# Kernel optimization log

Measured on AMD Instinct MI355X. Metric: run time of the kernel, lower is better.

Reference implementation:

```python
import jax, jax.numpy as jnp
import numpy as np


def _seg_softmax(e, seg, n):
    m = jax.ops.segment_max(e, seg, num_segments=n)
    ex = jnp.exp(e - m[seg])
    s = jax.ops.segment_sum(ex, seg, num_segments=n)
    return ex / (s[seg] + 1e-16)


def _gat_conv(x, src, dst, ea, W, a_s, a_d, We, a_e, b, heads, C, concat, N):
    # PyG GATConv math (eval mode, no dropout)
    h = (x @ W).reshape(N, heads, C)                    # [N,H,C]
    he = (ea @ We).reshape(-1, heads, C)                # [Ef,H,C]
    al = jnp.sum(h * a_s, -1)[src] + jnp.sum(h * a_d, -1)[dst] + jnp.sum(he * a_e, -1)
    al = jax.nn.leaky_relu(al, 0.2)                     # [Ef,H]
    alpha = _seg_softmax(al, dst, N)
    out = jax.ops.segment_sum(alpha[:, :, None] * h[src], dst, num_segments=N)
    out = out.reshape(N, heads * C) if concat else out.mean(1)
    return out + b


def _ln(x, g, b):
    mu = x.mean(-1, keepdims=True)
    v = x.var(-1, keepdims=True)
    return (x - mu) / jnp.sqrt(v + 1e-5) * g + b


def setup_inputs() -> dict:
    key = jax.random.key(0)
    ks = jax.random.split(key, 20)
    B, L, E_PER = 512, 64, 4
    N = B * L
    E = N * E_PER
    x = jax.random.normal(ks[0], (N, 55), jnp.float32)
    # within-graph random edges (each graph is a contiguous block of L nodes)
    off = (jnp.arange(E) // (L * E_PER)) * L
    src = off + jax.random.randint(ks[1], (E,), 0, L)
    dst = off + jax.random.randint(ks[2], (E,), 0, L)
    edge_index = jnp.stack([src, dst])
    edge_attr = jax.random.uniform(ks[3], (E, 6), dtype=jnp.float32)
    node_gid = jnp.arange(N) // L
    food_ids = jax.random.randint(ks[4], (B,), 0, 29)
    p = lambda i, shape: jax.random.normal(ks[i], shape, jnp.float32) * 0.05
    return dict(
        x=x, edge_attr=edge_attr, edge_index=edge_index, node_gid=node_gid, food_ids=food_ids,
        W1=p(5, (55, 1024)), as1=p(6, (4, 256)), ad1=p(7, (4, 256)),
        We1=p(8, (6, 1024)), ae1=p(9, (4, 256)), b1=jnp.zeros((1024,), jnp.float32),
        g1=jnp.ones((1024,), jnp.float32), be1=jnp.zeros((1024,), jnp.float32),
        W2=p(10, (1024, 256)), as2=p(11, (1, 256)), ad2=p(12, (1, 256)),
        We2=p(13, (6, 256)), ae2=p(14, (1, 256)), b2=jnp.zeros((256,), jnp.float32),
        g2=jnp.ones((256,), jnp.float32), be2=jnp.zeros((256,), jnp.float32),
        Wa=p(15, (256, 256)), va=p(16, (256,)), emb=p(17, (29, 256)))


def reference(x, edge_attr, edge_index, node_gid, food_ids,
              W1, as1, ad1, We1, ae1, b1, g1, be1,
              W2, as2, ad2, We2, ae2, b2, g2, be2,
              Wa, va, emb):
    N = x.shape[0]
    B = food_ids.shape[0]
    src, dst = edge_index[0], edge_index[1]
    # add self loops; self-loop edge_attr = mean of incoming edge attrs (PyG fill_value='mean')
    ones = jnp.ones((src.shape[0],), x.dtype)
    deg = jax.ops.segment_sum(ones, dst, num_segments=N)
    mean_ea = jax.ops.segment_sum(edge_attr, dst, num_segments=N) / jnp.maximum(deg, 1.0)[:, None]
    loop = jnp.arange(N)
    src_f = jnp.concatenate([src, loop])
    dst_f = jnp.concatenate([dst, loop])
    ea_f = jnp.concatenate([edge_attr, mean_ea], 0)
    # GATEncoder
    h = _gat_conv(x, src_f, dst_f, ea_f, W1, as1, ad1, We1, ae1, b1, 4, 256, True, N)
    h = jax.nn.relu(_ln(h, g1, be1))
    h = _gat_conv(h, src_f, dst_f, ea_f, W2, as2, ad2, We2, ae2, b2, 1, 256, False, N)
    h = _ln(h, g2, be2)                                  # [N,256]
    # per-graph attention over nodes, then attention-weighted max-pool
    scores = jnp.tanh(h @ Wa) @ va                       # [N]
    attn = _seg_softmax(scores, node_gid, B)             # [N]
    hw = h * attn[:, None]
    drug_fea = jax.ops.segment_max(hw, node_gid, num_segments=B)[:, None, :]  # [B,1,256]
    food_fea = emb[food_ids][:, None, :]                 # [B,1,256]
    return drug_fea, food_fea, attn
```

## Files before the change

### kernel.cpp

```cpp
#include <hip/hip_runtime.h>
#include <cstdint>
#include <cstddef>


#define LEAKY_SLOPE 0.2f

typedef __attribute__((ext_vector_type(8))) _Float16 half8;
typedef __attribute__((ext_vector_type(4))) float facc4;

__global__ void k_prep_w(const float* __restrict__ W1, const float* __restrict__ W2,
                         const float* __restrict__ Wa,
                         const float* __restrict__ We1, const float* __restrict__ ae1,
                         const float* __restrict__ We2, const float* __restrict__ ae2,
                         const float* __restrict__ as1, const float* __restrict__ ad1,
                         _Float16* __restrict__ w1f, _Float16* __restrict__ w2t,
                         _Float16* __restrict__ wat, float* __restrict__ fold) {
    int idx = blockIdx.x * blockDim.x + threadIdx.x;
    if (idx < 1024 * 64) {
        int head = idx >> 14;
        int rem = idx & 16383;
        int c = rem >> 6, k = rem & 63;
        _Float16 v = (k < 55) ? (_Float16)W1[(size_t)k * 1024 + head * 256 + c]
                              : (_Float16)0.f;
        int dst = head * 16384 + ((c >> 4) * 2 + (k >> 5)) * 512 +
                  ((c & 15) + 16 * ((k >> 3) & 3)) * 8 + (k & 7);
        w1f[dst] = v;
        return;
    }
    idx -= 1024 * 64;
    if (idx < 256 * 1024) {
        int c = idx >> 10, k = idx & 1023;
        w2t[idx] = (_Float16)W2[(size_t)k * 256 + c];
        return;
    }
    idx -= 256 * 1024;
    if (idx < 256 * 256) {
        int c = idx >> 8, k = idx & 255;
        int dst = ((c >> 4) * 8 + (k >> 5)) * 512 + ((c & 15) + 16 * ((k >> 3) & 3)) * 8 + (k & 7);
        wat[dst] = (_Float16)Wa[(size_t)k * 256 + c];
        return;
    }
    int t = idx - 256 * 256;
    if (t < 24) {
        int k = t >> 2, h = t & 3;
        float s = 0.f;
        for (int c = 0; c < 256; ++c) s += We1[k * 1024 + h * 256 + c] * ae1[h * 256 + c];
        fold[t] = s;
    } else if (t < 30) {
        int k = t - 24;
        float s = 0.f;
        for (int c = 0; c < 256; ++c) s += We2[k * 256 + c] * ae2[c];
        fold[32 + k] = s;
    } else if (t >= 64 && t < 284) {
        int i = t - 64, k = i >> 2, h = i & 3;
        float s = 0.f;
        for (int c = 0; c < 256; ++c) s += W1[k * 1024 + h * 256 + c] * as1[h * 256 + c];
        fold[64 + i] = s;
    } else if (t >= 320 && t < 540) {
        int i = t - 320, k = i >> 2, h = i & 3;
        float s = 0.f;
        for (int c = 0; c < 256; ++c) s += W1[k * 1024 + h * 256 + c] * ad1[h * 256 + c];
        fold[320 + i] = s;
    }
}

__global__ void k_prep_x(const float* __restrict__ x, const float* __restrict__ wa1,
                         const float* __restrict__ wd1, _Float16* __restrict__ xbf,
                         float* __restrict__ ss1, float* __restrict__ sd1, int N) {
    int idx = blockIdx.x * blockDim.x + threadIdx.x;
    if (idx < N * 64) {
        int n = idx >> 6, k = idx & 63;
        _Float16 v = (k < 55) ? (_Float16)x[(size_t)n * 55 + k] : (_Float16)0.f;
        int g = n >> 6, nl = n & 63;
        size_t dst = (size_t)g * 4096 +
                     (((k >> 4) * 2 + (nl >> 5)) * 512 +
                      ((k & 15) + 16 * ((nl >> 3) & 3)) * 8 + (nl & 7));
        xbf[dst] = v;
        return;
    }
    int n = idx - N * 64;
    if (n >= N) return;
    float a0 = 0, a1 = 0, a2 = 0, a3 = 0, d0 = 0, d1 = 0, d2 = 0, d3 = 0;
    for (int k = 0; k < 55; ++k) {
        float xv = x[(size_t)n * 55 + k];
        float4 wa = *reinterpret_cast<const float4*>(&wa1[k * 4]);
        float4 wd = *reinterpret_cast<const float4*>(&wd1[k * 4]);
        a0 += xv * wa.x; a1 += xv * wa.y; a2 += xv * wa.z; a3 += xv * wa.w;
        d0 += xv * wd.x; d1 += xv * wd.y; d2 += xv * wd.z; d3 += xv * wd.w;
    }
    *reinterpret_cast<float4*>(&ss1[n * 4]) = make_float4(a0, a1, a2, a3);
    *reinterpret_cast<float4*>(&sd1[n * 4]) = make_float4(d0, d1, d2, d3);
}

__global__ __launch_bounds__(256) void k_graph_csr(
    const int* __restrict__ ei, const float* __restrict__ ea,
    const float* __restrict__ we1, const float* __restrict__ we2,
    int* __restrict__ coff, int* __restrict__ eid,
    float* __restrict__ ead1, float* __restrict__ ead2, int E, int B) {
    __shared__ int degL[64];
    __shared__ float meaL[64][6];
    __shared__ int cs[65];
    __shared__ int fillL[64];
    int g = blockIdx.x;
    int ng = g * 64;
    int e0 = g * 256;
    int tid = threadIdx.x;
    if (tid < 64) {
        degL[tid] = 0; fillL[tid] = 0;
#pragma unroll
        for (int k = 0; k < 6; ++k) meaL[tid][k] = 0.f;
    }
    __syncthreads();
    int eg = e0 + tid;
    int dst = ei[E + eg];
    int dl = dst - ng;
    atomicAdd(&degL[dl], 1);
#pragma unroll
    for (int k = 0; k < 6; ++k) atomicAdd(&meaL[dl][k], ea[(size_t)eg * 6 + k]);
    __syncthreads();
    if (tid < 64) {
        int v = degL[tid] + 1;
        int incl = v;
#pragma unroll
        for (int o = 1; o < 64; o <<= 1) {
            int up = __shfl_up(incl, o);
            if (tid >= o) incl += up;
        }
        cs[tid + 1] = incl;
        if (tid == 0) cs[0] = 0;
        coff[ng + tid] = g * 320 + (incl - v);
        if (g == B - 1 && tid == 63) coff[ng + 64] = (g + 1) * 320;
    }
    __syncthreads();
    {
        float v[4] = {};
        float v2 = 0.f;
        const float* eap = ea + (size_t)eg * 6;
#pragma unroll
        for (int k = 0; k < 6; ++k) {
            float a = eap[k];
#pragma unroll
            for (int h = 0; h < 4; ++h) v[h] += a * we1[k * 4 + h];
            v2 += a * we2[k];
        }
#pragma unroll
        for (int h = 0; h < 4; ++h) ead1[(size_t)eg * 4 + h] = v[h];
        ead2[eg] = v2;
        int pos = cs[dl] + atomicAdd(&fillL[dl], 1);
        eid[g * 320 + pos] = eg;
    }
    if (tid < 64) {
        float inv = 1.f / fmaxf((float)degL[tid], 1.f);
        float v[4] = {};
        float v2 = 0.f;
#pragma unroll
        for (int k = 0; k < 6; ++k) {
            float a = meaL[tid][k] * inv;
#pragma unroll
            for (int h = 0; h < 4; ++h) v[h] += a * we1[k * 4 + h];
            v2 += a * we2[k];
        }
        int se = E + ng + tid;
#pragma unroll
        for (int h = 0; h < 4; ++h) ead1[(size_t)se * 4 + h] = v[h];
        ead2[se] = v2;
        int pos = cs[tid] + atomicAdd(&fillL[tid], 1);
        eid[g * 320 + pos] = se;
    }
}

__global__ __launch_bounds__(512) void k_layer1(
    const _Float16* __restrict__ xbf,
    const int* __restrict__ coff, const int* __restrict__ eid, const int* __restrict__ ei,
    const float* __restrict__ ead1, const float* __restrict__ ss1,
    const float* __restrict__ sd1,
    const _Float16* __restrict__ w1f, _Float16* __restrict__ hpre,
    int E, int g0) {
    __shared__ _Float16 Pm[4][4096];
    __shared__ float llds[384][4];
    __shared__ int slds[384];
    _Float16* XAf = &Pm[0][0];
    int g = blockIdx.x;
    int ng = (g0 + g) * 64;
    int tid = threadIdx.x;
    int lane = tid & 63, wid = tid >> 6;
    int l15 = lane & 15, l4 = lane >> 4;
    for (int i = tid; i < 4 * 4096 / 8; i += 512)
        *reinterpret_cast<int4*>(&Pm[0][0] + i * 8) = int4{0, 0, 0, 0};
    int pbase = coff[ng];
    int pcnt = coff[ng + 64] - pbase;
    if (pcnt > 384) pcnt = 384;
    for (int p = tid; p < pcnt; p += 512) {
        int e = eid[pbase + p];
        int s, d;
        if (e < E) { s = ei[e]; d = ei[E + e]; } else { s = e - E; d = s; }
        slds[p] = s - ng;
        float4 sv = *reinterpret_cast<const float4*>(&ss1[s * 4]);
        float4 dv = *reinterpret_cast<const float4*>(&sd1[d * 4]);
        float4 ev = *reinterpret_cast<const float4*>(&ead1[(size_t)e * 4]);
        float v0 = sv.x + dv.x + ev.x, v1 = sv.y + dv.y + ev.y;
        float v2 = sv.z + dv.z + ev.z, v3 = sv.w + dv.w + ev.w;
        llds[p][0] = (v0 > 0.f) ? v0 : LEAKY_SLOPE * v0;
        llds[p][1] = (v1 > 0.f) ? v1 : LEAKY_SLOPE * v1;
        llds[p][2] = (v2 > 0.f) ? v2 : LEAKY_SLOPE * v2;
        llds[p][3] = (v3 > 0.f) ? v3 : LEAKY_SLOPE * v3;
    }
    __syncthreads();
    if (tid < 256) {
        int dst = tid >> 2, h = tid & 3;
        int p0 = coff[ng + dst] - pbase, p1 = coff[ng + dst + 1] - pbase;
        float m = -1e30f;
        for (int p = p0; p < p1; ++p) m = fmaxf(m, llds[p][h]);
        float sm = 0.f;
        for (int p = p0; p < p1; ++p) sm += expf(llds[p][h] - m);
        float iv = 1.f / (sm + 1e-16f);
        for (int p = p0; p < p1; ++p) {
            int src = slds[p];
            int pos = dst * 64 + (((src >> 3) ^ (dst & 7)) << 3) + (src & 7);
            Pm[h][pos] = (_Float16)((float)Pm[h][pos] + expf(llds[p][h] - m) * iv);
        }
    }
    __syncthreads();
    int head = wid >> 1, fjh = wid & 1;
    const _Float16* xg = xbf + (size_t)(g0 + g) * 4096;
    facc4 acc1[4][2] = {};
#pragma unroll
    for (int kk = 0; kk < 2; ++kk) {
        half8 af[4], bf[2];
#pragma unroll
        for (int f = 0; f < 4; ++f) {
            int arow = f * 16 + l15;
            af[f] = *reinterpret_cast<const half8*>(
                &Pm[head][arow * 64 + (((kk * 4 + l4) ^ (arow & 7)) << 3)]);
        }
#pragma unroll
        for (int f = 0; f < 2; ++f)
            bf[f] = *reinterpret_cast<const half8*>(
                xg + (((fjh * 2 + f) * 2 + kk) * 512 + lane * 8));
#pragma unroll
        for (int fi = 0; fi < 4; ++fi)
#pragma unroll
            for (int fj = 0; fj < 2; ++fj)
                acc1[fi][fj] = __builtin_amdgcn_mfma_f32_16x16x32_f16(
                    af[fi], bf[fj], acc1[fi][fj], 0, 0, 0);
    }
    __syncthreads();
#pragma unroll
    for (int fi = 0; fi < 4; ++fi)
#pragma unroll
        for (int fj = 0; fj < 2; ++fj)
#pragma unroll
            for (int i = 0; i < 4; ++i) {
                int rl = l4 * 4 + i;
                int dst = head * 4096 + (fi * 2 + fjh) * 512 +
                          ((fj * 2 + (l15 >> 3)) * 16 + rl) * 8 + (l15 & 7);
                XAf[dst] = (_Float16)acc1[fi][fj][i];
            }
    __syncthreads();
    int hw = wid >> 1, ch = wid & 1;
    facc4 acc2[4][8] = {};
#pragma unroll
    for (int kk = 0; kk < 2; ++kk) {
        half8 af[4], bf[8];
#pragma unroll
        for (int f = 0; f < 4; ++f)
            af[f] = *reinterpret_cast<const half8*>(
                &XAf[hw * 4096 + (f * 2 + kk) * 512 + lane * 8]);
#pragma unroll
        for (int f = 0; f < 8; ++f)
            bf[f] = *reinterpret_cast<const half8*>(
                w1f + hw * 16384 + ((ch * 8 + f) * 2 + kk) * 512 + lane * 8);
#pragma unroll
        for (int fi = 0; fi < 4; ++fi)
#pragma unroll
            for (int fj = 0; fj < 8; ++fj)
                acc2[fi][fj] = __builtin_amdgcn_mfma_f32_16x16x32_f16(
                    af[fi], bf[fj], acc2[fi][fj], 0, 0, 0);
    }
#pragma unroll
    for (int fi = 0; fi < 4; ++fi)
#pragma unroll
        for (int fj = 0; fj < 8; ++fj)
#pragma unroll
            for (int i = 0; i < 4; ++i) {
                int r = g * 64 + fi * 16 + l4 * 4 + i;
                int cc = hw * 256 + ch * 128 + fj * 16 + l15;
                hpre[(size_t)r * 1024 + cc] = (_Float16)acc2[fi][fj][i];
            }
}

__global__ __launch_bounds__(256) void k_ln1(
    const _Float16* __restrict__ hpre, const float* __restrict__ b1,
    const float* __restrict__ g1, const float* __restrict__ be1,
    _Float16* __restrict__ hln) {
    int row = blockIdx.x * 4 + (threadIdx.x >> 6);
    int lane = threadIdx.x & 63;
    const _Float16* src = hpre + (size_t)row * 1024;
    float v[16];
    half8 h0 = *reinterpret_cast<const half8*>(src + lane * 8);
    half8 h1 = *reinterpret_cast<const half8*>(src + 512 + lane * 8);
    float lsum = 0.f, lsq = 0.f;
#pragma unroll
    for (int j = 0; j < 8; ++j) {
        v[j] = (float)h0[j] + b1[lane * 8 + j];
        v[8 + j] = (float)h1[j] + b1[512 + lane * 8 + j];
    }
#pragma unroll
    for (int j = 0; j < 16; ++j) { lsum += v[j]; lsq += v[j] * v[j]; }
    for (int o = 32; o; o >>= 1) { lsum += __shfl_xor(lsum, o); lsq += __shfl_xor(lsq, o); }
    float mu = lsum * (1.f / 1024.f);
    float var = lsq * (1.f / 1024.f) - mu * mu;
    float rstd = rsqrtf(var + 1e-5f);
    half8 o0, o1;
#pragma unroll
    for (int j = 0; j < 8; ++j) {
        int c = lane * 8 + j;
        o0[j] = (_Float16)fmaxf((v[j] - mu) * rstd * g1[c] + be1[c], 0.f);
    }
#pragma unroll
    for (int j = 0; j < 8; ++j) {
        int c = 512 + lane * 8 + j;
        o1[j] = (_Float16)fmaxf((v[8 + j] - mu) * rstd * g1[c] + be1[c], 0.f);
    }
    *reinterpret_cast<half8*>(hln + (size_t)row * 1024 + lane * 8) = o0;
    *reinterpret_cast<half8*>(hln + (size_t)row * 1024 + 512 + lane * 8) = o1;
}

__global__ __launch_bounds__(512) void k_gemm2(
    const _Float16* __restrict__ A, const _Float16* __restrict__ BT,
    _Float16* __restrict__ h2f) {
    __shared__ _Float16 As[128 * 64];
    __shared__ _Float16 Bs[256 * 64];
    int tid = threadIdx.x;
    int lane = tid & 63, wid = tid >> 6;
    int wr = wid >> 2, wc = wid & 3;
    int l15 = lane & 15, l4 = lane >> 4;
    int r0 = blockIdx.x * 128;
    facc4 acc[4][4] = {};
    for (int kt = 0; kt < 1024; kt += 64) {
#pragma unroll
        for (int i = 0; i < 2; ++i) {
            int ch = tid + 512 * i;
            int row = ch >> 3, col16 = ch & 7;
            int sw = col16 ^ (row & 7);
            *reinterpret_cast<int4*>(&As[row * 64 + sw * 8]) =
                *reinterpret_cast<const int4*>(A + (size_t)(r0 + row) * 1024 + kt + col16 * 8);
        }
#pragma unroll
        for (int i = 0; i < 4; ++i) {
            int ch = tid + 512 * i;
            int row = ch >> 3, col16 = ch & 7;
            int sw = col16 ^ (row & 7);
            *reinterpret_cast<int4*>(&Bs[row * 64 + sw * 8]) =
                *reinterpret_cast<const int4*>(BT + (size_t)row * 1024 + kt + col16 * 8);
        }
        __syncthreads();
#pragma unroll
        for (int kk = 0; kk < 2; ++kk) {
            half8 af[4], bf[4];
#pragma unroll
            for (int f = 0; f < 4; ++f) {
                int arow = wr * 64 + f * 16 + l15;
                int ac = (kk * 4 + l4) ^ (arow & 7);
                af[f] = *reinterpret_cast<const half8*>(&As[arow * 64 + ac * 8]);
                int brow = wc * 64 + f * 16 + l15;
                int bc = (kk * 4 + l4) ^ (brow & 7);
                bf[f] = *reinterpret_cast<const half8*>(&Bs[brow * 64 + bc * 8]);
            }
#pragma unroll
            for (int fi = 0; fi < 4; ++fi)
#pragma unroll
                for (int fj = 0; fj < 4; ++fj)
                    acc[fi][fj] = __builtin_amdgcn_mfma_f32_16x16x32_f16(
                        af[fi], bf[fj], acc[fi][fj], 0, 0, 0);
        }
        __syncthreads();
    }
#pragma unroll
    for (int fi = 0; fi < 4; ++fi)
#pragma unroll
        for (int fj = 0; fj < 4; ++fj)
#pragma unroll
            for (int i = 0; i < 4; ++i) {
                int r = r0 + wr * 64 + fi * 16 + l4 * 4 + i;
                int cc = wc * 64 + fj * 16 + l15;
                int g = r >> 6, nl = r & 63;
                size_t dst = (size_t)g * 16384 +
                             (((cc >> 4) * 2 + (nl >> 5)) * 512 +
                              ((cc & 15) + 16 * ((nl >> 3) & 3)) * 8 + (nl & 7));
                h2f[dst] = (_Float16)acc[fi][fj][i];
            }
}

__global__ __launch_bounds__(512) void k_graph2f(
    const _Float16* __restrict__ h2f,
    const int* __restrict__ coff, const int* __restrict__ eid, const int* __restrict__ ei,
    const float* __restrict__ ead2, const float* __restrict__ as2,
    const float* __restrict__ ad2,
    const float* __restrict__ b2, const float* __restrict__ g2,
    const float* __restrict__ be2,
    const _Float16* __restrict__ wat, const float* __restrict__ va,
    const int* __restrict__ food, const float* __restrict__ emb,
    float* __restrict__ out, int E, int B, int g0) {
    __shared__ _Float16 hfL[64 * 256];
    _Float16* Pm = hfL;
    float* llds = reinterpret_cast<float*>(hfL + 4096);
    int* slds = reinterpret_cast<int*>(hfL + 4096 + 768);
    __shared__ float rsum[64], rsq[64], ss2L[64], sd2L[64];
    __shared__ float part[8][64];
    __shared__ float at[64];
    int g = blockIdx.x;
    int b = g0 + g;
    int ng = (g0 + g) * 64;
    int tid = threadIdx.x;
    int lane = tid & 63, wid = tid >> 6;
    int l15 = lane & 15, l4 = lane >> 4;
    int cbase = wid * 32;
    if (tid < 64) { rsum[tid] = 0.f; rsq[tid] = 0.f; ss2L[tid] = 0.f; sd2L[tid] = 0.f; }
    for (int i = tid; i < 64 * 64 / 8; i += 512)
        *reinterpret_cast<int4*>(&Pm[0] + i * 8) = int4{0, 0, 0, 0};
    __syncthreads();
    const _Float16* hg = h2f + (size_t)g * 16384;
    half8 bfr[2][2];
#pragma unroll
    for (int kk = 0; kk < 2; ++kk)
#pragma unroll
        for (int f = 0; f < 2; ++f)
            bfr[kk][f] = *reinterpret_cast<const half8*>(
                hg + ((((cbase + f * 16) >> 4) * 2 + kk) * 512 + lane * 8));
    float ps[2][8] = {}, pd[2][8] = {};
#pragma unroll
    for (int kk = 0; kk < 2; ++kk)
#pragma unroll
        for (int f = 0; f < 2; ++f) {
            int c = cbase + f * 16 + l15;
            float a2 = as2[c], d2 = ad2[c];
#pragma unroll
            for (int j = 0; j < 8; ++j) {
                float hv = (float)bfr[kk][f][j];
                ps[kk][j] += hv * a2;
                pd[kk][j] += hv * d2;
            }
        }
#pragma unroll
    for (int kk = 0; kk < 2; ++kk)
#pragma unroll
        for (int j = 0; j < 8; ++j) {
            float s = ps[kk][j], d = pd[kk][j];
            s += __shfl_xor(s, 1); d += __shfl_xor(d, 1);
            s += __shfl_xor(s, 2); d += __shfl_xor(d, 2);
            s += __shfl_xor(s, 4); d += __shfl_xor(d, 4);
            s += __shfl_xor(s, 8); d += __shfl_xor(d, 8);
            if (l15 == 0) {
                int n = kk * 32 + l4 * 8 + j;
                atomicAdd(&ss2L[n], s);
                atomicAdd(&sd2L[n], d);
            }
        }
    __syncthreads();
    int pbase = coff[ng];
    int pcnt = coff[ng + 64] - pbase;
    if (pcnt > 384) pcnt = 384;
    for (int p = tid; p < pcnt; p += 512) {
        int e = eid[pbase + p];
        int s, d;
        if (e < E) { s = ei[e]; d = ei[E + e]; } else { s = e - E; d = s; }
        slds[p] = s - ng;
        float v = ss2L[s - ng] + sd2L[d - ng] + ead2[e];
        llds[p] = (v > 0.f) ? v : LEAKY_SLOPE * v;
    }
    __syncthreads();
    if (tid < 64) {
        int dst = tid;
        int p0 = coff[ng + dst] - pbase, p1 = coff[ng + dst + 1] - pbase;
        float m = -1e30f;
        for (int p = p0; p < p1; ++p) m = fmaxf(m, llds[p]);
        float sm = 0.f;
        for (int p = p0; p < p1; ++p) sm += expf(llds[p] - m);
        float iv = 1.f / (sm + 1e-16f);
        for (int p = p0; p < p1; ++p) {
            int src = slds[p];
            int pos = dst * 64 + (((src >> 3) ^ (dst & 7)) << 3) + (src & 7);
            Pm[pos] = (_Float16)((float)Pm[pos] + expf(llds[p] - m) * iv);
        }
    }
    __syncthreads();
    facc4 acc[4][2] = {};
#pragma unroll
    for (int kk = 0; kk < 2; ++kk) {
        half8 af[4];
#pragma unroll
        for (int f = 0; f < 4; ++f) {
            int arow = f * 16 + l15;
            af[f] = *reinterpret_cast<const half8*>(
                &Pm[arow * 64 + (((kk * 4 + l4) ^ (arow & 7)) << 3)]);
        }
#pragma unroll
        for (int fi = 0; fi < 4; ++fi)
#pragma unroll
            for (int fj = 0; fj < 2; ++fj)
                acc[fi][fj] = __builtin_amdgcn_mfma_f32_16x16x32_f16(
                    af[fi], bfr[kk][fj], acc[fi][fj], 0, 0, 0);
    }
    float bb[2];
#pragma unroll
    for (int fj = 0; fj < 2; ++fj) bb[fj] = b2[cbase + fj * 16 + l15];
#pragma unroll
    for (int fi = 0; fi < 4; ++fi)
#pragma unroll
        for (int i = 0; i < 4; ++i) {
            float s = 0.f, q = 0.f;
#pragma unroll
            for (int fj = 0; fj < 2; ++fj) {
                float v = acc[fi][fj][i] + bb[fj];
                acc[fi][fj][i] = v;
                s += v; q += v * v;
            }
            s += __shfl_xor(s, 1); q += __shfl_xor(q, 1);
            s += __shfl_xor(s, 2); q += __shfl_xor(q, 2);
            s += __shfl_xor(s, 4); q += __shfl_xor(q, 4);
            s += __shfl_xor(s, 8); q += __shfl_xor(q, 8);
            if (l15 == 0) {
                int r = fi * 16 + l4 * 4 + i;
                atomicAdd(&rsum[r], s);
                atomicAdd(&rsq[r], q);
            }
        }
    __syncthreads();
#pragma unroll
    for (int fi = 0; fi < 4; ++fi)
#pragma unroll
        for (int i = 0; i < 4; ++i) {
            int rl = l4 * 4 + i;
            float mu = rsum[fi * 16 + rl] * (1.f / 256.f);
            float var = rsq[fi * 16 + rl] * (1.f / 256.f) - mu * mu;
            float rstd = rsqrtf(var + 1e-5f);
#pragma unroll
            for (int fj = 0; fj < 2; ++fj) {
                int c = cbase + fj * 16 + l15;
                float v = (acc[fi][fj][i] - mu) * rstd * g2[c] + be2[c];
                acc[fi][fj][i] = v;
                int idx = (fi * 8 + wid) * 512 +
                          ((fj * 2 + (l15 >> 3)) * 16 + rl) * 8 + (l15 & 7);
                hfL[idx] = (_Float16)v;
            }
        }
    __syncthreads();
    facc4 acc2[4][2] = {};
#pragma unroll
    for (int kk = 0; kk < 8; ++kk) {
        half8 af[4], bf[2];
#pragma unroll
        for (int f = 0; f < 4; ++f)
            af[f] = *reinterpret_cast<const half8*>(&hfL[(f * 8 + kk) * 512 + lane * 8]);
#pragma unroll
        for (int f = 0; f < 2; ++f)
            bf[f] = *reinterpret_cast<const half8*>(
                wat + (((wid * 2 + f) * 8 + kk) * 512 + lane * 8));
#pragma unroll
        for (int fi = 0; fi < 4; ++fi)
#pragma unroll
            for (int fj = 0; fj < 2; ++fj)
                acc2[fi][fj] = __builtin_amdgcn_mfma_f32_16x16x32_f16(
                    af[fi], bf[fj], acc2[fi][fj], 0, 0, 0);
    }
    float vac[2];
#pragma unroll
    for (int fj = 0; fj < 2; ++fj) vac[fj] = va[cbase + fj * 16 + l15];
#pragma unroll
    for (int fi = 0; fi < 4; ++fi)
#pragma unroll
        for (int i = 0; i < 4; ++i) {
            float v = tanhf(acc2[fi][0][i]) * vac[0] + tanhf(acc2[fi][1][i]) * vac[1];
            v += __shfl_xor(v, 1); v += __shfl_xor(v, 2);
            v += __shfl_xor(v, 4); v += __shfl_xor(v, 8);
            if (l15 == 0) part[wid][fi * 16 + l4 * 4 + i] = v;
        }
    __syncthreads();
    if (tid < 64) {
        float sc = part[0][tid] + part[1][tid] + part[2][tid] + part[3][tid] +
                   part[4][tid] + part[5][tid] + part[6][tid] + part[7][tid];
        float m = sc;
        for (int o = 32; o; o >>= 1) m = fmaxf(m, __shfl_xor(m, o));
        float ex = expf(sc - m);
        float s = ex;
        for (int o = 32; o; o >>= 1) s += __shfl_xor(s, o);
        float a = ex / (s + 1e-16f);
        at[tid] = a;
        out[(size_t)B * 512 + (size_t)b * 64 + tid] = a;
    }
    __syncthreads();
#pragma unroll
    for (int fj = 0; fj < 2; ++fj) {
        float m = -1e30f;
#pragma unroll
        for (int fi = 0; fi < 4; ++fi)
#pragma unroll
            for (int i = 0; i < 4; ++i) {
                int r = fi * 16 + l4 * 4 + i;
                m = fmaxf(m, acc[fi][fj][i] * at[r]);
            }
        m = fmaxf(m, __shfl_xor(m, 16));
        m = fmaxf(m, __shfl_xor(m, 32));
        if (l4 == 0)
            out[(size_t)b * 256 + cbase + fj * 16 + l15] = m;
    }
    if (tid < 256)
        out[(size_t)B * 256 + (size_t)b * 256 + tid] =
            emb[(size_t)food[b] * 256 + tid];
}

extern "C" void kernel_launch(void* const* d_in, const int* in_sizes, int n_in,
                              void* d_out, int out_size, void* d_ws, size_t ws_size,
                              hipStream_t stream) {
    const float* x   = (const float*)d_in[0];
    const float* ea  = (const float*)d_in[1];
    const int*   ei  = (const int*)d_in[2];
    const int*   food= (const int*)d_in[4];
    const float* W1  = (const float*)d_in[5];
    const float* as1 = (const float*)d_in[6];
    const float* ad1 = (const float*)d_in[7];
    const float* We1 = (const float*)d_in[8];
    const float* ae1 = (const float*)d_in[9];
    const float* b1  = (const float*)d_in[10];
    const float* g1  = (const float*)d_in[11];
    const float* be1 = (const float*)d_in[12];
    const float* W2  = (const float*)d_in[13];
    const float* as2 = (const float*)d_in[14];
    const float* ad2 = (const float*)d_in[15];
    const float* We2 = (const float*)d_in[16];
    const float* ae2 = (const float*)d_in[17];
    const float* b2  = (const float*)d_in[18];
    const float* g2  = (const float*)d_in[19];
    const float* be2 = (const float*)d_in[20];
    const float* Wa  = (const float*)d_in[21];
    const float* va  = (const float*)d_in[22];
    const float* emb = (const float*)d_in[23];
    float* out = (float*)d_out;

    const int N  = in_sizes[0] / 55;
    const int E  = in_sizes[2] / 2;
    const int B  = in_sizes[4];
    const int Ef = E + N;
    const int LPG = N / B;

    char* w = (char*)d_ws;
    size_t off = 0;
    auto take = [&](size_t bytes) -> char* {
        char* p = w + off;
        off = (off + bytes + 255) & ~(size_t)255;
        return p;
    };
    int*      coff = (int*)take((size_t)(N + 1) * 4);
    int*      eid  = (int*)take((size_t)Ef * 4);
    float*    ead1 = (float*)take((size_t)Ef * 4 * 4);
    float*    ead2 = (float*)take((size_t)Ef * 4);
    float*    fold = (float*)take(4096 * 4);
    float*    ss1  = (float*)take((size_t)N * 4 * 4);
    float*    sd1  = (float*)take((size_t)N * 4 * 4);
    _Float16* xbf  = (_Float16*)take((size_t)N * 64 * 2);
    _Float16* w1f  = (_Float16*)take((size_t)1024 * 64 * 2);
    _Float16* w2t  = (_Float16*)take((size_t)256 * 1024 * 2);
    _Float16* wat  = (_Float16*)take((size_t)256 * 256 * 2);
    size_t smallEnd = off;

    int G = B;
    while (G > 2 && smallEnd + 2ull * G * 131072 + 768 > ws_size) G >>= 1;
    _Float16* hpre = (_Float16*)take((size_t)G * 131072);
    _Float16* hln  = (_Float16*)take((size_t)G * 131072);
    _Float16* h2f  = (_Float16*)hpre;

    k_prep_w<<<(1024 * 64 + 256 * 1024 + 256 * 256 + 3072 + 255) / 256, 256, 0, stream>>>(
        W1, W2, Wa, We1, ae1, We2, ae2, as1, ad1, w1f, w2t, wat, fold);
    k_prep_x<<<(N * 64 + N + 255) / 256, 256, 0, stream>>>(
        x, fold + 64, fold + 320, xbf, ss1, sd1, N);
    k_graph_csr<<<B, 256, 0, stream>>>(ei, ea, fold, fold + 32, coff, eid,
                                       ead1, ead2, E, B);

    for (int g0 = 0; g0 < B; g0 += G) {
        int Gc = (g0 + G <= B) ? G : (B - g0);
        int NC = Gc * LPG;
        k_layer1<<<Gc, 512, 0, stream>>>(xbf, coff, eid, ei, ead1, ss1, sd1,
                                         w1f, hpre, E, g0);
        k_ln1<<<NC / 4, 256, 0, stream>>>(hpre, b1, g1, be1, hln);
        k_gemm2<<<NC / 128, 512, 0, stream>>>(hln, w2t, h2f);
        k_graph2f<<<Gc, 512, 0, stream>>>(h2f, coff, eid, ei, ead2, as2, ad2,
                                          b2, g2, be2, wat, va, food, emb,
                                          out, E, B, g0);
    }
}
```

Baseline: 148.5 us.

## Fuse bias+LayerNorm+ReLU into layer1 epilogue and store MFMA-fragment layout for gemm2

Layer-1's epilogue now adds the bias, reduces row sums and sums of squares across waves through shared-memory atomics, and applies LayerNorm and ReLU in registers. It writes the result in the fragment-packed layout that gemm2 reads directly from global memory. This removes the separate k_ln1 kernel, one fp16 round trip of the 1024-wide activation, and gemm2's A-tile staging in shared memory. The costs are scattered 2-byte stores in the epilogue, an extra barrier, and gemm2 A loads that go uncached straight from global.

```diff
diff --git a/kernel.cpp b/kernel.cpp
--- a/kernel.cpp
+++ b/kernel.cpp
@@ -174,17 +174,21 @@
     const int* __restrict__ coff, const int* __restrict__ eid, const int* __restrict__ ei,
     const float* __restrict__ ead1, const float* __restrict__ ss1,
     const float* __restrict__ sd1,
-    const _Float16* __restrict__ w1f, _Float16* __restrict__ hpre,
-    int E, int g0) {
+    const _Float16* __restrict__ w1f,
+    const float* __restrict__ b1, const float* __restrict__ g1,
+    const float* __restrict__ be1,
+    _Float16* __restrict__ hlnf, int E, int g0) {
     __shared__ _Float16 Pm[4][4096];
     __shared__ float llds[384][4];
     __shared__ int slds[384];
+    __shared__ float rsum[64], rsq[64];
     _Float16* XAf = &Pm[0][0];
     int g = blockIdx.x;
     int ng = (g0 + g) * 64;
     int tid = threadIdx.x;
     int lane = tid & 63, wid = tid >> 6;
     int l15 = lane & 15, l4 = lane >> 4;
+    if (tid < 64) { rsum[tid] = 0.f; rsq[tid] = 0.f; }
     for (int i = tid; i < 4 * 4096 / 8; i += 512)
         *reinterpret_cast<int4*>(&Pm[0][0] + i * 8) = int4{0, 0, 0, 0};
     int pbase = coff[ng];
@@ -258,6 +262,7 @@
             }
     __syncthreads();
     int hw = wid >> 1, ch = wid & 1;
+    int cbase = hw * 256 + ch * 128;
     facc4 acc2[4][8] = {};
 #pragma unroll
     for (int kk = 0; kk < 2; ++kk) {
@@ -277,75 +282,64 @@
                 acc2[fi][fj] = __builtin_amdgcn_mfma_f32_16x16x32_f16(
                     af[fi], bf[fj], acc2[fi][fj], 0, 0, 0);
     }
+    float bb[8];
+#pragma unroll
+    for (int fj = 0; fj < 8; ++fj) bb[fj] = b1[cbase + fj * 16 + l15];
 #pragma unroll
     for (int fi = 0; fi < 4; ++fi)
 #pragma unroll
-        for (int fj = 0; fj < 8; ++fj)
-#pragma unroll
-            for (int i = 0; i < 4; ++i) {
-                int r = g * 64 + fi * 16 + l4 * 4 + i;
-                int cc = hw * 256 + ch * 128 + fj * 16 + l15;
-                hpre[(size_t)r * 1024 + cc] = (_Float16)acc2[fi][fj][i];
-            }
+        for (int i = 0; i < 4; ++i) {
+            float s = 0.f, q = 0.f;
+#pragma unroll
+            for (int fj = 0; fj < 8; ++fj) {
+                float v = acc2[fi][fj][i] + bb[fj];
+                acc2[fi][fj][i] = v;
+                s += v; q += v * v;
+            }
+            s += __shfl_xor(s, 1); q += __shfl_xor(q, 1);
+            s += __shfl_xor(s, 2); q += __shfl_xor(q, 2);
+            s += __shfl_xor(s, 4); q += __shfl_xor(q, 4);
+            s += __shfl_xor(s, 8); q += __shfl_xor(q, 8);
+            if (l15 == 0) {
+                int r = fi * 16 + l4 * 4 + i;
+                atomicAdd(&rsum[r], s);
+                atomicAdd(&rsq[r], q);
+            }
+        }
+    __syncthreads();
+#pragma unroll
+    for (int fi = 0; fi < 4; ++fi)
+#pragma unroll
+        for (int i = 0; i < 4; ++i) {
+            int rl = l4 * 4 + i;
+            int r = fi * 16 + rl;
+            float mu = rsum[r] * (1.f / 1024.f);
+            float var = rsq[r] * (1.f / 1024.f) - mu * mu;
+            float rstd = rsqrtf(var + 1e-5f);
+#pragma unroll
+            for (int fj = 0; fj < 8; ++fj) {
+                int c = cbase + fj * 16 + l15;
+                float v = fmaxf((acc2[fi][fj][i] - mu) * rstd * g1[c] + be1[c], 0.f);
+                size_t dst = (size_t)g * 65536 +
+                             ((fi * 32 + (c >> 5)) * 512 +
+                              (rl + 16 * ((c >> 3) & 3)) * 8 + (c & 7));
+                hlnf[dst] = (_Float16)v;
+            }
+        }
 }
 
-__global__ __launch_bounds__(256) void k_ln1(
-    const _Float16* __restrict__ hpre, const float* __restrict__ b1,
-    const float* __restrict__ g1, const float* __restrict__ be1,
-    _Float16* __restrict__ hln) {
-    int row = blockIdx.x * 4 + (threadIdx.x >> 6);
-    int lane = threadIdx.x & 63;
-    const _Float16* src = hpre + (size_t)row * 1024;
-    float v[16];
-    half8 h0 = *reinterpret_cast<const half8*>(src + lane * 8);
-    half8 h1 = *reinterpret_cast<const half8*>(src + 512 + lane * 8);
-    float lsum = 0.f, lsq = 0.f;
-#pragma unroll
-    for (int j = 0; j < 8; ++j) {
-        v[j] = (float)h0[j] + b1[lane * 8 + j];
-        v[8 + j] = (float)h1[j] + b1[512 + lane * 8 + j];
-    }
-#pragma unroll
-    for (int j = 0; j < 16; ++j) { lsum += v[j]; lsq += v[j] * v[j]; }
-    for (int o = 32; o; o >>= 1) { lsum += __shfl_xor(lsum, o); lsq += __shfl_xor(lsq, o); }
-    float mu = lsum * (1.f / 1024.f);
-    float var = lsq * (1.f / 1024.f) - mu * mu;
-    float rstd = rsqrtf(var + 1e-5f);
-    half8 o0, o1;
-#pragma unroll
-    for (int j = 0; j < 8; ++j) {
-        int c = lane * 8 + j;
-        o0[j] = (_Float16)fmaxf((v[j] - mu) * rstd * g1[c] + be1[c], 0.f);
-    }
-#pragma unroll
-    for (int j = 0; j < 8; ++j) {
-        int c = 512 + lane * 8 + j;
-        o1[j] = (_Float16)fmaxf((v[8 + j] - mu) * rstd * g1[c] + be1[c], 0.f);
-    }
-    *reinterpret_cast<half8*>(hln + (size_t)row * 1024 + lane * 8) = o0;
-    *reinterpret_cast<half8*>(hln + (size_t)row * 1024 + 512 + lane * 8) = o1;
-}
-
 __global__ __launch_bounds__(512) void k_gemm2(
-    const _Float16* __restrict__ A, const _Float16* __restrict__ BT,
+    const _Float16* __restrict__ hlnf, const _Float16* __restrict__ BT,
     _Float16* __restrict__ h2f) {
-    __shared__ _Float16 As[128 * 64];
     __shared__ _Float16 Bs[256 * 64];
     int tid = threadIdx.x;
     int lane = tid & 63, wid = tid >> 6;
     int wr = wid >> 2, wc = wid & 3;
     int l15 = lane & 15, l4 = lane >> 4;
     int r0 = blockIdx.x * 128;
+    const _Float16* Ag = hlnf + (size_t)(r0 / 64 + wr) * 65536;
     facc4 acc[4][4] = {};
     for (int kt = 0; kt < 1024; kt += 64) {
-#pragma unroll
-        for (int i = 0; i < 2; ++i) {
-            int ch = tid + 512 * i;
-            int row = ch >> 3, col16 = ch & 7;
-            int sw = col16 ^ (row & 7);
-            *reinterpret_cast<int4*>(&As[row * 64 + sw * 8]) =
-                *reinterpret_cast<const int4*>(A + (size_t)(r0 + row) * 1024 + kt + col16 * 8);
-        }
 #pragma unroll
         for (int i = 0; i < 4; ++i) {
             int ch = tid + 512 * i;
@@ -357,12 +351,12 @@
         __syncthreads();
 #pragma unroll
         for (int kk = 0; kk < 2; ++kk) {
+            int ks = (kt >> 5) + kk;
             half8 af[4], bf[4];
 #pragma unroll
             for (int f = 0; f < 4; ++f) {
-                int arow = wr * 64 + f * 16 + l15;
-                int ac = (kk * 4 + l4) ^ (arow & 7);
-                af[f] = *reinterpret_cast<const half8*>(&As[arow * 64 + ac * 8]);
+                af[f] = *reinterpret_cast<const half8*>(
+                    Ag + (f * 32 + ks) * 512 + lane * 8);
                 int brow = wc * 64 + f * 16 + l15;
                 int bc = (kk * 4 + l4) ^ (brow & 7);
                 bf[f] = *reinterpret_cast<const half8*>(&Bs[brow * 64 + bc * 8]);
@@ -665,10 +659,10 @@
     size_t smallEnd = off;
 
     int G = B;
-    while (G > 2 && smallEnd + 2ull * G * 131072 + 768 > ws_size) G >>= 1;
-    _Float16* hpre = (_Float16*)take((size_t)G * 131072);
-    _Float16* hln  = (_Float16*)take((size_t)G * 131072);
-    _Float16* h2f  = (_Float16*)hpre;
+    while (G > 2 && smallEnd + (size_t)G * 131072 + (size_t)G * 32768 + 768 > ws_size)
+        G >>= 1;
+    _Float16* hlnf = (_Float16*)take((size_t)G * 131072);
+    _Float16* h2f  = (_Float16*)take((size_t)G * 32768);
 
     k_prep_w<<<(1024 * 64 + 256 * 1024 + 256 * 256 + 3072 + 255) / 256, 256, 0, stream>>>(
         W1, W2, Wa, We1, ae1, We2, ae2, as1, ad1, w1f, w2t, wat, fold);
@@ -681,9 +675,8 @@
         int Gc = (g0 + G <= B) ? G : (B - g0);
         int NC = Gc * LPG;
         k_layer1<<<Gc, 512, 0, stream>>>(xbf, coff, eid, ei, ead1, ss1, sd1,
-                                         w1f, hpre, E, g0);
-        k_ln1<<<NC / 4, 256, 0, stream>>>(hpre, b1, g1, be1, hln);
-        k_gemm2<<<NC / 128, 512, 0, stream>>>(hln, w2t, h2f);
+                                         w1f, b1, g1, be1, hlnf, E, g0);
+        k_gemm2<<<NC / 128, 512, 0, stream>>>(hlnf, w2t, h2f);
         k_graph2f<<<Gc, 512, 0, stream>>>(h2f, coff, eid, ei, ead2, as2, ad2,
                                           b2, g2, be2, wat, va, food, emb,
                                           out, E, B, g0);
```

After: 151.1 us. About the same (+1.7%).
